# Kernel optimization log

Measured on AMD Instinct MI355X. Metric: run time of the kernel, lower is better.

Reference implementation:

```python
import jax, jax.numpy as jnp
import numpy as np

N = 50000      # nodes
E = 400000     # lower-adjacency edges (avg degree 8)
D = 128        # input_dim == output_dim (o_dim in DEC_HOGNN)
GEO = 20       # geo_dim
H = 3          # heads
C = 128        # out_channels per head
NUM_LAYERS = 3


def _lin_init(key, fan_in, fan_out, extra=()):
    s = 1.0 / np.sqrt(fan_in)
    return jax.random.uniform(key, extra + (fan_in, fan_out), jnp.float32, -s, s)


def setup_inputs() -> dict:
    key = jax.random.key(0)
    ks = jax.random.split(key, 20)
    inp = {
        "h": jax.random.normal(ks[0], (N, D), jnp.float32),
        "lower_adj_feat": jax.random.normal(ks[1], (E, GEO), jnp.float32),
        "dir_w": jax.random.normal(ks[2], (E, 1), jnp.float32),
        "src_idx": jax.random.randint(ks[3], (E,), 0, N),
        "dst_idx": jax.random.randint(ks[4], (E,), 0, N),
        # edge_encoder: Linear(2*D + geo + 1 -> D)
        "W_ee": _lin_init(ks[5], 2 * D + GEO + 1, D),
        "b_ee": jnp.zeros((D,), jnp.float32),
        # residual linear (layer 0 only; others Identity)
        "W_res": _lin_init(ks[6], D, D),
        "b_res": jnp.zeros((D,), jnp.float32),
        # 3 TransformerConv layers, all in=D out=C heads=H (stacked)
        "Wq": _lin_init(ks[7], D, H * C, (NUM_LAYERS,)),
        "bq": jnp.zeros((NUM_LAYERS, H * C), jnp.float32),
        "Wk": _lin_init(ks[8], D, H * C, (NUM_LAYERS,)),
        "bk": jnp.zeros((NUM_LAYERS, H * C), jnp.float32),
        "Wv": _lin_init(ks[9], D, H * C, (NUM_LAYERS,)),
        "bv": jnp.zeros((NUM_LAYERS, H * C), jnp.float32),
        "We": _lin_init(ks[10], D, H * C, (NUM_LAYERS,)),
        "be": jnp.zeros((NUM_LAYERS, H * C), jnp.float32),
        # lin_skip: in -> out_channels (concat=False)
        "Ws": _lin_init(ks[11], D, C, (NUM_LAYERS,)),
        "bs": jnp.zeros((NUM_LAYERS, C), jnp.float32),
        # ctr_lin: Linear(input_dim + output_dim -> output_dim)
        "W_ctr": _lin_init(ks[12], 2 * D, D),
        "b_ctr": jnp.zeros((D,), jnp.float32),
    }
    return inp


def _transformer_conv(x, src, dst, e_attr, Wq, bq, Wk, bk, Wv, bv, We, be, Ws, bs):
    """PyG TransformerConv, heads=H, concat=False (head mean), root skip."""
    n = x.shape[0]
    q = (x @ Wq + bq).reshape(n, H, C)
    k = (x @ Wk + bk).reshape(n, H, C)
    v = (x @ Wv + bv).reshape(n, H, C)
    e = (e_attr @ We + be).reshape(-1, H, C)      # [E,H,C]
    ke = k[src] + e                                # edge-conditioned keys
    alpha = (q[dst] * ke).sum(-1) / jnp.sqrt(jnp.asarray(C, x.dtype))  # [E,H]
    # segment softmax over destination nodes
    amax = jax.ops.segment_max(alpha, dst, num_segments=n)
    amax = jnp.where(jnp.isfinite(amax), amax, 0.0)
    ex = jnp.exp(alpha - amax[dst])
    den = jax.ops.segment_sum(ex, dst, num_segments=n)
    w = ex / (den[dst] + 1e-16)
    msg = (v[src] + e) * w[:, :, None]             # [E,H,C]
    out = jax.ops.segment_sum(msg.reshape(-1, H * C), dst, num_segments=n)
    out = out.reshape(n, H, C).mean(axis=1)        # concat=False -> head mean
    return out + x @ Ws + bs                       # root weight skip


def reference(h, lower_adj_feat, dir_w, src_idx, dst_idx,
              W_ee, b_ee, W_res, b_res,
              Wq, bq, Wk, bk, Wv, bv, We, be, Ws, bs,
              W_ctr, b_ctr):
    # edge encoder: [h[dst], h[src]*dir, dir, geo] -> D
    edge_features = jnp.concatenate(
        [h[dst_idx], h[src_idx] * dir_w, dir_w, lower_adj_feat], axis=-1)
    edge_attr = edge_features @ W_ee + b_ee
    h_cur = h
    for i in range(NUM_LAYERS):
        residual = (h_cur @ W_res + b_res) if i == 0 else h_cur
        h_t = _transformer_conv(h_cur, src_idx, dst_idx, edge_attr,
                                Wq[i], bq[i], Wk[i], bk[i], Wv[i], bv[i],
                                We[i], be[i], Ws[i], bs[i])
        h_cur = jax.nn.relu(h_t + residual)
    return jnp.concatenate([h, h_cur], axis=-1) @ W_ctr + b_ctr
```

## Files before the change

### kernel.cpp

```cpp
#include <hip/hip_runtime.h>
#include <math.h>

#define NN 50000
#define NE 400000

typedef _Float16 f16;
typedef _Float16 f16x8 __attribute__((ext_vector_type(8)));
typedef _Float16 f16x4 __attribute__((ext_vector_type(4)));
typedef _Float16 f16x2 __attribute__((ext_vector_type(2)));
typedef float f32x4 __attribute__((ext_vector_type(4)));

static __device__ __forceinline__ float dot8(f16x8 a, f16x8 b, float acc) {
#if defined(__has_builtin) && __has_builtin(__builtin_amdgcn_fdot2)
#pragma unroll
  for (int j = 0; j < 4; ++j) {
    f16x2 x = {a[2 * j], a[2 * j + 1]};
    f16x2 y = {b[2 * j], b[2 * j + 1]};
    acc = __builtin_amdgcn_fdot2(x, y, acc, false);
  }
#else
#pragma unroll
  for (int j = 0; j < 8; ++j) acc += (float)a[j] * (float)b[j];
#endif
  return acc;
}

#if defined(__has_builtin) && __has_builtin(__builtin_amdgcn_global_load_lds)
#define HAVE_GLL 1
static __device__ __forceinline__ void gload_lds16(const f16* gp, f16* lp) {
  __builtin_amdgcn_global_load_lds((const __attribute__((address_space(1))) void*)gp,
                                   (__attribute__((address_space(3))) void*)lp, 16, 0, 0);
}
#else
#define HAVE_GLL 0
#endif

__global__ __launch_bounds__(256) void hgemm_k128_kernel(
    const f16* __restrict__ A, int lda,
    const f16* __restrict__ WT,
    const float* __restrict__ bias,
    f16* __restrict__ outb, int ldb,
    int M, int ntiles)
{
  __shared__ f16 As[128 * 128];
  __shared__ f16 Bs[64 * 128];
  const int t = threadIdx.x;
  const int wv = t >> 6, lane = t & 63;
  const int l15 = lane & 15, l4 = lane >> 4;
  const int c8 = lane & 15, rsub = lane >> 4;
  const int row0 = blockIdx.x * 128;

#if HAVE_GLL
#pragma unroll
  for (int k = 0; k < 8; ++k) {
    int r = wv * 4 + k * 16 + rsub;
    int rc = row0 + r; if (rc >= M) rc = M - 1;
    const f16* gp = A + (size_t)rc * lda + ((c8 ^ (r & 15)) << 3);
    gload_lds16(gp, As + (wv * 4 + k * 16) * 128);
  }
#else
  for (int i = t; i < 2048; i += 256) {
    int r = i >> 4, cc = i & 15;
    int gr = row0 + r; if (gr >= M) gr = M - 1;
    float4 v = *(const float4*)(A + (size_t)gr * lda + cc * 8);
    *(float4*)(As + r * 128 + ((cc ^ (r & 15)) << 3)) = v;
  }
#endif
  for (int ct = 0; ct < ntiles; ++ct) {
    const int col0 = (blockIdx.y * ntiles + ct) * 64;
#if HAVE_GLL
#pragma unroll
    for (int k = 0; k < 4; ++k) {
      int c = wv * 4 + k * 16 + rsub;
      const f16* gp = WT + (size_t)(col0 + c) * 128 + ((c8 ^ (c & 15)) << 3);
      gload_lds16(gp, Bs + (wv * 4 + k * 16) * 128);
    }
#else
    for (int i = t; i < 1024; i += 256) {
      int c = i >> 4, cc = i & 15;
      float4 v = *(const float4*)(WT + (size_t)(col0 + c) * 128 + cc * 8);
      *(float4*)(Bs + c * 128 + ((cc ^ (c & 15)) << 3)) = v;
    }
#endif
    __syncthreads();
    f32x4 acc[2][4];
#pragma unroll
    for (int m = 0; m < 2; ++m)
#pragma unroll
      for (int n = 0; n < 4; ++n) acc[m][n] = (f32x4){0.f, 0.f, 0.f, 0.f};
#pragma unroll
    for (int ks = 0; ks < 4; ++ks) {
      const int co = (((ks * 4 + l4) ^ l15) << 3);
      f16x8 a0 = *(const f16x8*)(As + (wv * 32 +      l15) * 128 + co);
      f16x8 a1 = *(const f16x8*)(As + (wv * 32 + 16 + l15) * 128 + co);
      f16x8 b0 = *(const f16x8*)(Bs + (     l15) * 128 + co);
      f16x8 b1 = *(const f16x8*)(Bs + (16 + l15) * 128 + co);
      f16x8 b2 = *(const f16x8*)(Bs + (32 + l15) * 128 + co);
      f16x8 b3 = *(const f16x8*)(Bs + (48 + l15) * 128 + co);
      acc[0][0] = __builtin_amdgcn_mfma_f32_16x16x32_f16(a0, b0, acc[0][0], 0, 0, 0);
      acc[0][1] = __builtin_amdgcn_mfma_f32_16x16x32_f16(a0, b1, acc[0][1], 0, 0, 0);
      acc[0][2] = __builtin_amdgcn_mfma_f32_16x16x32_f16(a0, b2, acc[0][2], 0, 0, 0);
      acc[0][3] = __builtin_amdgcn_mfma_f32_16x16x32_f16(a0, b3, acc[0][3], 0, 0, 0);
      acc[1][0] = __builtin_amdgcn_mfma_f32_16x16x32_f16(a1, b0, acc[1][0], 0, 0, 0);
      acc[1][1] = __builtin_amdgcn_mfma_f32_16x16x32_f16(a1, b1, acc[1][1], 0, 0, 0);
      acc[1][2] = __builtin_amdgcn_mfma_f32_16x16x32_f16(a1, b2, acc[1][2], 0, 0, 0);
      acc[1][3] = __builtin_amdgcn_mfma_f32_16x16x32_f16(a1, b3, acc[1][3], 0, 0, 0);
    }
    __syncthreads();
    float bv4[4];
#pragma unroll
    for (int n = 0; n < 4; ++n) bv4[n] = bias ? bias[col0 + n * 16 + l15] : 0.f;
#pragma unroll
    for (int m = 0; m < 2; ++m) {
#pragma unroll
      for (int j = 0; j < 4; ++j) {
        int r = row0 + wv * 32 + m * 16 + l4 * 4 + j;
        if (r >= M) continue;
#pragma unroll
        for (int n = 0; n < 4; ++n) {
          int c = col0 + n * 16 + l15;
          outb[(size_t)r * ldb + c] = (f16)(acc[m][n][j] + bv4[n]);
        }
      }
    }
  }
}

__global__ __launch_bounds__(256) void hgemm2_kernel(
    const f16* __restrict__ A, int lda,
    const f16* __restrict__ A2, int lda2, int a2k,
    const f16* __restrict__ WT, int K,
    const float* __restrict__ bias,
    f16* __restrict__ outb, int ldb,
    const f16* __restrict__ fresid, int ldr,
    int dorelu, int M,
    const f16* __restrict__ ctrW, const float* __restrict__ ctrB,
    float* __restrict__ ctrOut)
{
  __shared__ f16 As[128 * 128];
  __shared__ f16 Bs[128 * 128];
  const int t = threadIdx.x;
  const int wv = t >> 6, lane = t & 63;
  const int l15 = lane & 15, l4 = lane >> 4;
  const int c8 = lane & 15, rsub = lane >> 4;
  const int row0 = blockIdx.x * 128;
  const int col0 = blockIdx.y * 128;

  f32x4 acc[2][8];
#pragma unroll
  for (int m = 0; m < 2; ++m)
#pragma unroll
    for (int n = 0; n < 8; ++n) acc[m][n] = (f32x4){0.f, 0.f, 0.f, 0.f};

  for (int kc = 0; kc < K; kc += 128) {
    const f16* Ap; int koff, ldA;
    if (kc >= a2k) { Ap = A2; koff = kc - a2k; ldA = lda2; }
    else           { Ap = A;  koff = kc;       ldA = lda;  }
#if HAVE_GLL
#pragma unroll
    for (int k = 0; k < 8; ++k) {
      int r = wv * 4 + k * 16 + rsub;
      int rc = row0 + r; if (rc >= M) rc = M - 1;
      const f16* gp = Ap + (size_t)rc * ldA + koff + ((c8 ^ (r & 15)) << 3);
      gload_lds16(gp, As + (wv * 4 + k * 16) * 128);
    }
#pragma unroll
    for (int k = 0; k < 8; ++k) {
      int c = wv * 4 + k * 16 + rsub;
      const f16* gp = WT + (size_t)(col0 + c) * K + kc + ((c8 ^ (c & 15)) << 3);
      gload_lds16(gp, Bs + (wv * 4 + k * 16) * 128);
    }
#else
    for (int i = t; i < 2048; i += 256) {
      int r = i >> 4, cc = i & 15;
      int gr = row0 + r; if (gr >= M) gr = M - 1;
      float4 v = *(const float4*)(Ap + (size_t)gr * ldA + koff + cc * 8);
      *(float4*)(As + r * 128 + ((cc ^ (r & 15)) << 3)) = v;
    }
    for (int i = t; i < 2048; i += 256) {
      int c = i >> 4, cc = i & 15;
      float4 v = *(const float4*)(WT + (size_t)(col0 + c) * K + kc + cc * 8);
      *(float4*)(Bs + c * 128 + ((cc ^ (c & 15)) << 3)) = v;
    }
#endif
    __syncthreads();
#pragma unroll
    for (int ks = 0; ks < 4; ++ks) {
      const int co = (((ks * 4 + l4) ^ l15) << 3);
      f16x8 a0 = *(const f16x8*)(As + (wv * 32 +      l15) * 128 + co);
      f16x8 a1 = *(const f16x8*)(As + (wv * 32 + 16 + l15) * 128 + co);
#pragma unroll
      for (int n = 0; n < 8; ++n) {
        f16x8 b = *(const f16x8*)(Bs + (n * 16 + l15) * 128 + co);
        acc[0][n] = __builtin_amdgcn_mfma_f32_16x16x32_f16(a0, b, acc[0][n], 0, 0, 0);
        acc[1][n] = __builtin_amdgcn_mfma_f32_16x16x32_f16(a1, b, acc[1][n], 0, 0, 0);
      }
    }
    __syncthreads();
  }

  float bv8[8];
#pragma unroll
  for (int n = 0; n < 8; ++n) bv8[n] = bias ? bias[col0 + n * 16 + l15] : 0.f;
#pragma unroll
  for (int m = 0; m < 2; ++m) {
#pragma unroll
    for (int j = 0; j < 4; ++j) {
      int rl = wv * 32 + m * 16 + l4 * 4 + j;
      int r = row0 + rl;
#pragma unroll
      for (int n = 0; n < 8; ++n) {
        int c = col0 + n * 16 + l15;
        float val = acc[m][n][j] + bv8[n];
        if (fresid) val += (float)fresid[(size_t)r * ldr + c];
        if (dorelu) val = fmaxf(val, 0.f);
        f16 hv = (f16)val;
        if (r < M) outb[(size_t)r * ldb + c] = hv;
        if (ctrOut)
          As[rl * 128 + (((c >> 3) ^ (rl & 15)) << 3) + (c & 7)] = hv;
      }
    }
  }

  if (ctrOut) {
    for (int i = t; i < 2048; i += 256) {
      int c = i >> 4, k8 = i & 15;
      float4 v = *(const float4*)(ctrW + (size_t)c * 256 + k8 * 8);
      *(float4*)(Bs + c * 128 + ((k8 ^ (c & 15)) << 3)) = v;
    }
    __syncthreads();
    f32x4 acc2[2][8];
#pragma unroll
    for (int m = 0; m < 2; ++m)
#pragma unroll
      for (int n = 0; n < 8; ++n) acc2[m][n] = (f32x4){0.f, 0.f, 0.f, 0.f};
#pragma unroll
    for (int ks = 0; ks < 4; ++ks) {
      const int co = (((ks * 4 + l4) ^ l15) << 3);
      f16x8 a0 = *(const f16x8*)(As + (wv * 32 +      l15) * 128 + co);
      f16x8 a1 = *(const f16x8*)(As + (wv * 32 + 16 + l15) * 128 + co);
#pragma unroll
      for (int n = 0; n < 8; ++n) {
        f16x8 b = *(const f16x8*)(Bs + (n * 16 + l15) * 128 + co);
        acc2[0][n] = __builtin_amdgcn_mfma_f32_16x16x32_f16(a0, b, acc2[0][n], 0, 0, 0);
        acc2[1][n] = __builtin_amdgcn_mfma_f32_16x16x32_f16(a1, b, acc2[1][n], 0, 0, 0);
      }
    }
    __syncthreads();
    for (int i = t; i < 2048; i += 256) {
      int r = i >> 4, k8 = i & 15;
      int gr = row0 + r; if (gr >= M) gr = M - 1;
      float4 v = *(const float4*)(A2 + (size_t)gr * lda2 + 128 + k8 * 8);
      *(float4*)(As + r * 128 + ((k8 ^ (r & 15)) << 3)) = v;
    }
    for (int i = t; i < 2048; i += 256) {
      int c = i >> 4, k8 = i & 15;
      float4 v = *(const float4*)(ctrW + (size_t)c * 256 + 128 + k8 * 8);
      *(float4*)(Bs + c * 128 + ((k8 ^ (c & 15)) << 3)) = v;
    }
    __syncthreads();
#pragma unroll
    for (int ks = 0; ks < 4; ++ks) {
      const int co = (((ks * 4 + l4) ^ l15) << 3);
      f16x8 a0 = *(const f16x8*)(As + (wv * 32 +      l15) * 128 + co);
      f16x8 a1 = *(const f16x8*)(As + (wv * 32 + 16 + l15) * 128 + co);
#pragma unroll
      for (int n = 0; n < 8; ++n) {
        f16x8 b = *(const f16x8*)(Bs + (n * 16 + l15) * 128 + co);
        acc2[0][n] = __builtin_amdgcn_mfma_f32_16x16x32_f16(a0, b, acc2[0][n], 0, 0, 0);
        acc2[1][n] = __builtin_amdgcn_mfma_f32_16x16x32_f16(a1, b, acc2[1][n], 0, 0, 0);
      }
    }
#pragma unroll
    for (int m = 0; m < 2; ++m) {
#pragma unroll
      for (int j = 0; j < 4; ++j) {
        int r = row0 + wv * 32 + m * 16 + l4 * 4 + j;
        if (r >= M) continue;
#pragma unroll
        for (int n = 0; n < 8; ++n) {
          int c = n * 16 + l15;
          ctrOut[(size_t)r * 128 + c] = acc2[m][n][j] + ctrB[c];
        }
      }
    }
  }
}

__global__ void zero_int_kernel(int* __restrict__ p, int n) {
  int i = blockIdx.x * 256 + threadIdx.x;
  if (i < n) p[i] = 0;
}
__global__ void hist_kernel(const int* __restrict__ dst, int* __restrict__ deg) {
  int e = blockIdx.x * 256 + threadIdx.x;
  if (e < NE) atomicAdd(&deg[dst[e]], 1);
}
__global__ void scanA_kernel(const int* __restrict__ deg, int* __restrict__ rowstart,
                             int* __restrict__ part) {
  __shared__ int sd[256];
  int b = blockIdx.x, t = threadIdx.x, i = b * 256 + t;
  sd[t] = (i < NN) ? deg[i] : 0;
  __syncthreads();
  for (int o = 1; o < 256; o <<= 1) {
    int v = (t >= o) ? sd[t - o] : 0;
    __syncthreads();
    sd[t] += v;
    __syncthreads();
  }
  if (i < NN) rowstart[i + 1] = sd[t];
  if (t == 255) part[b] = sd[255];
}
__global__ void scanB_kernel(int* __restrict__ part, int nb) {
  __shared__ int sd[256];
  int t = threadIdx.x;
  sd[t] = (t < nb) ? part[t] : 0;
  __syncthreads();
  for (int o = 1; o < 256; o <<= 1) {
    int v = (t >= o) ? sd[t - o] : 0;
    __syncthreads();
    sd[t] += v;
    __syncthreads();
  }
  if (t < nb) part[t] = sd[t];
}
__global__ void scanC_kernel(const int* __restrict__ deg, int* __restrict__ rowstart,
                             const int* __restrict__ part, int* __restrict__ cursor) {
  int b = blockIdx.x, t = threadIdx.x, i = b * 256 + t;
  if (i >= NN) return;
  int off = b ? part[b - 1] : 0;
  int fin = rowstart[i + 1] + off;
  rowstart[i + 1] = fin;
  cursor[i] = fin - deg[i];
  if (i == 0) rowstart[0] = 0;
}
__global__ void scatter_kernel(const int* __restrict__ dst, const int* __restrict__ src,
                               const float* __restrict__ dirw, const float* __restrict__ geo,
                               int* __restrict__ cursor,
                               int* __restrict__ srcp, f16* __restrict__ dirpb,
                               f16* __restrict__ geop) {
  int e = blockIdx.x * 256 + threadIdx.x;
  if (e < NE) {
    int pos = atomicAdd(&cursor[dst[e]], 1);
    srcp[pos] = src[e];
    float dv = dirw[e];
    dirpb[pos] = (f16)dv;
    f16* gp = geop + (size_t)pos * 24;
#pragma unroll
    for (int j = 0; j < 20; ++j) gp[j] = (f16)geo[(size_t)e * 20 + j];
    gp[20] = (f16)dv;
    gp[21] = (f16)0.f; gp[22] = (f16)0.f; gp[23] = (f16)0.f;
  }
}

__global__ void prep_kernel(const float* __restrict__ Wee, const float* __restrict__ bee,
                            const float* __restrict__ WeAll, const float* __restrict__ beAll,
                            float* __restrict__ matsAll)
{
  const int layer = blockIdx.y;
  const float* We = WeAll + (size_t)layer * 49152;
  const float* be = beAll + (size_t)layer * 384;
  float* mats = matsAll + (size_t)layer * 132352;
  int idx = blockIdx.x * 256 + threadIdx.x;
  if (idx >= 132352) return;
  float acc = 0.0f;
  if (idx < 49152) {
    int h = idx >> 14, rem = idx & 16383, c = rem >> 7, u = rem & 127;
    for (int j = 0; j < 128; ++j)
      acc += We[(size_t)j * 384 + h * 128 + c] * Wee[(size_t)(128 + u) * 128 + j];
    mats[idx] = acc;
  } else if (idx < 58368) {
    int r = idx - 49152; int h = r / 3072; int rem = r - h * 3072; int c = rem / 24; int u = rem - c * 24;
    if (u < 21) {
      int trow = (u < 20) ? (257 + u) : 256;
      for (int j = 0; j < 128; ++j)
        acc += We[(size_t)j * 384 + h * 128 + c] * Wee[(size_t)trow * 128 + j];
    }
    mats[idx] = acc;
  } else if (idx < 107520) {
    int r = idx - 58368; int h = r >> 14; int rem = r & 16383; int tt = rem >> 7; int c = rem & 127;
    for (int j = 0; j < 128; ++j)
      acc += Wee[(size_t)(128 + tt) * 128 + j] * We[(size_t)j * 384 + h * 128 + c];
    mats[idx] = acc;
  } else if (idx < 115584) {
    int r = idx - 107520; int h = r / 2688; int rem = r - h * 2688; int tt = rem >> 7; int c = rem & 127;
    int trow = (tt < 20) ? (257 + tt) : 256;
    for (int j = 0; j < 128; ++j)
      acc += Wee[(size_t)trow * 128 + j] * We[(size_t)j * 384 + h * 128 + c];
    mats[idx] = acc;
  } else if (idx < 115968) {
    int r = idx - 115584; int h = r >> 7; int c = r & 127;
    for (int j = 0; j < 128; ++j)
      acc += bee[j] * We[(size_t)j * 384 + h * 128 + c];
    mats[idx] = acc + be[h * 128 + c];
  } else {
    int r = idx - 115968; int tt = r >> 7; int c = r & 127;
    for (int j = 0; j < 128; ++j)
      acc += Wee[(size_t)tt * 128 + j] *
             (We[(size_t)j * 384 + c] + We[(size_t)j * 384 + 128 + c] + We[(size_t)j * 384 + 256 + c]);
    mats[idx] = acc * (1.0f / 3.0f);
  }
}

__global__ void prepB_kernel(const float* __restrict__ Wq, const float* __restrict__ bq,
                             const float* __restrict__ Wk, const float* __restrict__ matsAll,
                             f16* __restrict__ WABT, float* __restrict__ biasAB)
{
  int idx = blockIdx.x * 256 + threadIdx.x;
  if (idx < 344064) {
    int i = idx / 114688; int r = idx % 114688; int c = r >> 7; int k = r & 127;
    float acc = 0.f;
    if (c < 384) {
      int h = c >> 7, u = c & 127;
      const float* wq = Wq + ((size_t)i * 128 + k) * 384 + h * 128;
      const float* wk = Wk + ((size_t)i * 128 + u) * 384 + h * 128;
      for (int c2 = 0; c2 < 128; ++c2) acc += wq[c2] * wk[c2];
    } else if (c < 768) {
      int h = (c - 384) >> 7, u = (c - 384) & 127;
      const float* wq = Wq + ((size_t)i * 128 + k) * 384 + h * 128;
      const float* m2 = matsAll + (size_t)i * 132352 + h * 16384 + u;
      for (int c2 = 0; c2 < 128; ++c2) acc += wq[c2] * m2[c2 * 128];
    } else if (c < 840) {
      int h = (c - 768) / 24, tt = (c - 768) % 24;
      const float* wq = Wq + ((size_t)i * 128 + k) * 384 + h * 128;
      const float* m34 = matsAll + (size_t)i * 132352 + 49152 + h * 3072 + tt;
      for (int c2 = 0; c2 < 128; ++c2) acc += wq[c2] * m34[c2 * 24];
    }
    WABT[(size_t)i * 114688 + c * 128 + k] = (f16)acc;
  } else if (idx < 346752) {
    int r = idx - 344064; int i = r / 896; int c = r % 896;
    float acc = 0.f;
    if (c < 384) {
      int h = c >> 7, u = c & 127;
      const float* bqv = bq + i * 384 + h * 128;
      const float* wk = Wk + ((size_t)i * 128 + u) * 384 + h * 128;
      for (int c2 = 0; c2 < 128; ++c2) acc += bqv[c2] * wk[c2];
    } else if (c < 768) {
      int h = (c - 384) >> 7, u = (c - 384) & 127;
      const float* bqv = bq + i * 384 + h * 128;
      const float* m2 = matsAll + (size_t)i * 132352 + h * 16384 + u;
      for (int c2 = 0; c2 < 128; ++c2) acc += bqv[c2] * m2[c2 * 128];
    } else if (c < 840) {
      int h = (c - 768) / 24, tt = (c - 768) % 24;
      const float* bqv = bq + i * 384 + h * 128;
      const float* m34 = matsAll + (size_t)i * 132352 + 49152 + h * 3072 + tt;
      for (int c2 = 0; c2 < 128; ++c2) acc += bqv[c2] * m34[c2 * 24];
    }
    biasAB[i * 896 + c] = acc;
  }
}

__global__ void prep2_kernel(const float* __restrict__ matsAll, const float* __restrict__ Wv,
                             const float* __restrict__ bv, const float* __restrict__ Ws,
                             const float* __restrict__ Wres, f16* __restrict__ W2bigT)
{
  int idx = blockIdx.x * 256 + threadIdx.x;
  if (idx >= 442368) return;
  int i = idx / 147456; int r = idx % 147456; int c = r / 1152; int k = r % 1152;
  float v = 0.f;
  if (k < 384) {
    int h = k >> 7, tt = k & 127;
    v = matsAll[(size_t)i * 132352 + 58368 + h * 16384 + tt * 128 + c];
  } else if (k < 768) {
    int h = (k - 384) >> 7, u = (k - 384) & 127;
    v = Wv[((size_t)i * 128 + u) * 384 + h * 128 + c];
  } else if (k < 840) {
    int h = (k - 768) / 24, tt = (k - 768) % 24;
    if (tt < 21)       v = matsAll[(size_t)i * 132352 + 107520 + h * 2688 + tt * 128 + c];
    else if (tt == 21) v = matsAll[(size_t)i * 132352 + 115584 + h * 128 + c]
                         + bv[i * 384 + h * 128 + c];
  } else if (k < 896) {
    v = 0.f;
  } else if (k < 1024) {
    v = matsAll[(size_t)i * 132352 + 115968 + (k - 896) * 128 + c];
  } else {
    v = Ws[((size_t)i * 128 + (k - 1024)) * 128 + c];
    if (i == 0) v += Wres[(k - 1024) * 128 + c];
  }
  W2bigT[(size_t)i * 147456 + c * 1152 + k] = (f16)v;
}

__global__ void wprep_kernel(const float* __restrict__ Wctr, const float* __restrict__ bs,
                             const float* __restrict__ bres,
                             f16* __restrict__ WctrT2, float* __restrict__ bias0)
{
  int idx = blockIdx.x * 256 + threadIdx.x;
  if (idx < 32768) {
    int c = idx >> 8, k = idx & 255;
    float v = (k < 128) ? Wctr[(size_t)(128 + k) * 128 + c]
                        : Wctr[(size_t)(k - 128) * 128 + c];
    WctrT2[idx] = (f16)v;
  } else if (idx < 32896) {
    int c = idx - 32768;
    bias0[c] = bs[c] + bres[c];
  }
}

__global__ __launch_bounds__(256) void attn_kernel(
    const f16* __restrict__ xh,
    f16* __restrict__ nbuf,
    const int* __restrict__ rowstart,
    const int* __restrict__ srcp,
    const f16* __restrict__ dirpb,
    const f16* __restrict__ geop)
{
  const int sl = threadIdx.x & 15;
  const int n = blockIdx.x * 16 + (threadIdx.x >> 4);
  const float rsC = 0.088388347648318447f;
  f16* row = nbuf + (size_t)n * 1024;

  f16x8 qk[3], g2[3];
#pragma unroll
  for (int h = 0; h < 3; ++h) {
    qk[h] = *(const f16x8*)(row + h * 128 + sl * 8);
    g2[h] = *(const f16x8*)(row + 384 + h * 128 + sl * 8);
  }
  float g34a[3], g34c[3];
#pragma unroll
  for (int h = 0; h < 3; ++h) {
    g34a[h] = (float)row[768 + h * 24 + sl];
    g34c[h] = (sl < 8) ? (float)row[768 + h * 24 + 16 + sl] : 0.f;
  }
  float den[3] = {0.f, 0.f, 0.f};
  float F2[3][8], Fv[3][8];
#pragma unroll
  for (int h = 0; h < 3; ++h)
#pragma unroll
    for (int j = 0; j < 8; ++j) { F2[h][j] = 0.f; Fv[h][j] = 0.f; }
  float f34a[3] = {0.f, 0.f, 0.f}, f34c[3] = {0.f, 0.f, 0.f};

  const int beg = rowstart[n], end = rowstart[n + 1];
  int ii = beg;
  for (; ii + 1 < end; ii += 2) {
    const int s0 = srcp[ii], s1 = srcp[ii + 1];
    const float d0 = (float)dirpb[ii], d1 = (float)dirpb[ii + 1];
    const f16* p0 = xh + (size_t)s0 * 256 + sl * 8;
    const f16* p1 = xh + (size_t)s1 * 256 + sl * 8;
    f16x8 xv0 = *(const f16x8*)p0;
    f16x8 hv0 = *(const f16x8*)(p0 + 128);
    f16x8 xv1 = *(const f16x8*)p1;
    f16x8 hv1 = *(const f16x8*)(p1 + 128);
    const float gea0 = (float)geop[(size_t)ii * 24 + sl];
    const float geb0 = (sl < 8) ? (float)geop[(size_t)ii * 24 + 16 + sl] : 0.f;
    const float gea1 = (float)geop[(size_t)(ii + 1) * 24 + sl];
    const float geb1 = (sl < 8) ? (float)geop[(size_t)(ii + 1) * 24 + 16 + sl] : 0.f;

    float pa[6];
#pragma unroll
    for (int h = 0; h < 3; ++h) {
      pa[h]     = dot8(qk[h], xv0, 0.f) + d0 * dot8(g2[h], hv0, 0.f)
                + gea0 * g34a[h] + geb0 * g34c[h];
      pa[3 + h] = dot8(qk[h], xv1, 0.f) + d1 * dot8(g2[h], hv1, 0.f)
                + gea1 * g34a[h] + geb1 * g34c[h];
    }
#pragma unroll
    for (int off = 1; off < 16; off <<= 1) {
#pragma unroll
      for (int q = 0; q < 6; ++q) pa[q] += __shfl_xor(pa[q], off);
    }
    float w0[3], w1[3];
#pragma unroll
    for (int h = 0; h < 3; ++h) {
      w0[h] = __expf(pa[h] * rsC);
      w1[h] = __expf(pa[3 + h] * rsC);
      den[h] += w0[h] + w1[h];
    }
#pragma unroll
    for (int h = 0; h < 3; ++h) {
      const float wd0 = w0[h] * d0, wd1 = w1[h] * d1;
#pragma unroll
      for (int j = 0; j < 8; ++j) {
        F2[h][j] = fmaf(wd0, (float)hv0[j], fmaf(wd1, (float)hv1[j], F2[h][j]));
        Fv[h][j] = fmaf(w0[h], (float)xv0[j], fmaf(w1[h], (float)xv1[j], Fv[h][j]));
      }
      f34a[h] = fmaf(w0[h], gea0, fmaf(w1[h], gea1, f34a[h]));
      f34c[h] = fmaf(w0[h], geb0, fmaf(w1[h], geb1, f34c[h]));
    }
  }
  if (ii < end) {
    const int s0 = srcp[ii];
    const float d0 = (float)dirpb[ii];
    const f16* p0 = xh + (size_t)s0 * 256 + sl * 8;
    f16x8 xv0 = *(const f16x8*)p0;
    f16x8 hv0 = *(const f16x8*)(p0 + 128);
    const float gea0 = (float)geop[(size_t)ii * 24 + sl];
    const float geb0 = (sl < 8) ? (float)geop[(size_t)ii * 24 + 16 + sl] : 0.f;
    float pa[3];
#pragma unroll
    for (int h = 0; h < 3; ++h)
      pa[h] = dot8(qk[h], xv0, 0.f) + d0 * dot8(g2[h], hv0, 0.f)
            + gea0 * g34a[h] + geb0 * g34c[h];
#pragma unroll
    for (int off = 1; off < 16; off <<= 1) {
#pragma unroll
      for (int q = 0; q < 3; ++q) pa[q] += __shfl_xor(pa[q], off);
    }
#pragma unroll
    for (int h = 0; h < 3; ++h) {
      const float w = __expf(pa[h] * rsC);
      den[h] += w;
      const float wd = w * d0;
#pragma unroll
      for (int j = 0; j < 8; ++j) {
        F2[h][j] = fmaf(wd, (float)hv0[j], F2[h][j]);
        Fv[h][j] = fmaf(w, (float)xv0[j], Fv[h][j]);
      }
      f34a[h] = fmaf(w, gea0, f34a[h]);
      f34c[h] = fmaf(w, geb0, f34c[h]);
    }
  }

  float sc[3], swh[3];
#pragma unroll
  for (int h = 0; h < 3; ++h) {
    sc[h] = (1.f / 3.f) / (den[h] + 1e-16f);
    swh[h] = den[h] * sc[h];
  }
#pragma unroll
  for (int h = 0; h < 3; ++h) {
    f16x8 o1, o2;
#pragma unroll
    for (int j = 0; j < 8; ++j) {
      o1[j] = (f16)(F2[h][j] * sc[h]);
      o2[j] = (f16)(Fv[h][j] * sc[h]);
    }
    *(f16x8*)(row + h * 128 + sl * 8) = o1;
    *(f16x8*)(row + 384 + h * 128 + sl * 8) = o2;
  }
#pragma unroll
  for (int h = 0; h < 3; ++h) {
    row[768 + h * 24 + sl] = (f16)(f34a[h] * sc[h]);
    if (sl < 8) {
      float fcv = (sl == 5) ? swh[h] : f34c[h] * sc[h];
      row[768 + h * 24 + 16 + sl] = (f16)fcv;
    }
  }
  f16x8 ho = *(const f16x8*)(xh + (size_t)n * 256 + 128 + sl * 8);
  if (beg >= end) {
#pragma unroll
    for (int j = 0; j < 8; ++j) ho[j] = (f16)0.f;
  }
  *(f16x8*)(row + 896 + sl * 8) = ho;
}

__global__ void hconv_kernel(const float* __restrict__ src, f16* __restrict__ xh) {
  int i = blockIdx.x * 256 + threadIdx.x;
  if (i >= NN * 32) return;
  float4 a = ((const float4*)src)[i];
  f16x4 o;
  o[0] = (f16)a.x; o[1] = (f16)a.y; o[2] = (f16)a.z; o[3] = (f16)a.w;
  int r = i >> 5, c4 = i & 31;
  *(f16x4*)(xh + (size_t)r * 256 + c4 * 4) = o;
  *(f16x4*)(xh + (size_t)r * 256 + 128 + c4 * 4) = o;
}

extern "C" void kernel_launch(void* const* d_in, const int* in_sizes, int n_in,
                              void* d_out, int out_size, void* d_ws, size_t ws_size,
                              hipStream_t stream)
{
  (void)in_sizes; (void)n_in; (void)out_size; (void)ws_size;
  const float* h    = (const float*)d_in[0];
  const float* geo  = (const float*)d_in[1];
  const float* dirw = (const float*)d_in[2];
  const int*   src  = (const int*)d_in[3];
  const int*   dst  = (const int*)d_in[4];
  const float* Wee  = (const float*)d_in[5];
  const float* bee  = (const float*)d_in[6];
  const float* Wres = (const float*)d_in[7];
  const float* bres = (const float*)d_in[8];
  const float* Wq   = (const float*)d_in[9];
  const float* bq   = (const float*)d_in[10];
  const float* Wk   = (const float*)d_in[11];
  const float* bk   = (const float*)d_in[12];  (void)bk;
  const float* Wv   = (const float*)d_in[13];
  const float* bv   = (const float*)d_in[14];
  const float* We   = (const float*)d_in[15];
  const float* be   = (const float*)d_in[16];
  const float* Ws   = (const float*)d_in[17];
  const float* bs   = (const float*)d_in[18];
  const float* Wctr = (const float*)d_in[19];
  const float* bctr = (const float*)d_in[20];

  char* base = (char*)d_ws;
  size_t off = 0;
  auto take = [&](size_t bytes) -> char* {
    char* p = base + off;
    off += bytes;
    off = (off + 255) & ~(size_t)255;
    return p;
  };
  f16* nbuf     = (f16*)take((size_t)NN * 1024 * 2);
  f16* xh       = (f16*)take((size_t)NN * 256 * 2);
  float* mats   = (float*)take((size_t)3 * 132352 * 4);
  f16* WABT     = (f16*)take((size_t)3 * 114688 * 2);
  float* biasAB = (float*)take((size_t)3 * 896 * 4);
  f16* W2bigT   = (f16*)take((size_t)3 * 147456 * 2);
  f16* WctrT2   = (f16*)take(32768 * 2);
  float* bias0  = (float*)take(128 * 4);
  f16* dirpb    = (f16*)take((size_t)NE * 2);
  f16* geop     = (f16*)take((size_t)NE * 24 * 2);
  int* deg      = (int*)take((size_t)NN * 4);
  int* rowstart = (int*)take((size_t)(NN + 1) * 4);
  int* cursor   = (int*)take((size_t)NN * 4);
  int* srcp     = (int*)take((size_t)NE * 4);
  int* part     = (int*)take(256 * 4);

  zero_int_kernel<<<(NN + 255) / 256, 256, 0, stream>>>(deg, NN);
  hist_kernel<<<(NE + 255) / 256, 256, 0, stream>>>(dst, deg);
  scanA_kernel<<<196, 256, 0, stream>>>(deg, rowstart, part);
  scanB_kernel<<<1, 256, 0, stream>>>(part, 196);
  scanC_kernel<<<196, 256, 0, stream>>>(deg, rowstart, part, cursor);
  scatter_kernel<<<(NE + 255) / 256, 256, 0, stream>>>(dst, src, dirw, geo, cursor,
                                                       srcp, dirpb, geop);
  hconv_kernel<<<6250, 256, 0, stream>>>(h, xh);
  wprep_kernel<<<129, 256, 0, stream>>>(Wctr, bs, bres, WctrT2, bias0);
  prep_kernel<<<dim3(518, 3), 256, 0, stream>>>(Wee, bee, We, be, mats);
  prepB_kernel<<<(346752 + 255) / 256, 256, 0, stream>>>(Wq, bq, Wk, mats, WABT, biasAB);
  prep2_kernel<<<(442368 + 255) / 256, 256, 0, stream>>>(mats, Wv, bv, Ws, Wres, W2bigT);

  for (int i = 0; i < 3; ++i) {
    hgemm_k128_kernel<<<dim3(391, 2), 256, 0, stream>>>(xh, 256, WABT + (size_t)i * 114688,
        biasAB + (size_t)i * 896, nbuf, 1024, NN, 7);
    attn_kernel<<<3125, 256, 0, stream>>>(xh, nbuf, rowstart, srcp, dirpb, geop);
    const float* obias = (i == 0) ? bias0 : (bs + i * 128);
    const f16* resid = (i == 0) ? nullptr : xh;
    const f16* ctrW = (i == 2) ? WctrT2 : nullptr;
    const float* ctrB = (i == 2) ? bctr : nullptr;
    float* ctrOut = (i == 2) ? (float*)d_out : nullptr;
    hgemm2_kernel<<<dim3(391, 1), 256, 0, stream>>>(nbuf, 1024, xh, 256, 1024,
        W2bigT + (size_t)i * 147456, 1152, obias, xh, 256,
        resid, 256, 1, NN, ctrW, ctrB, ctrOut);
  }
}
```

Before: 602.5 us.

## Compute weight-folding prep products with MFMA GEMMs instead of scalar loops

Replaces the scalar per-thread weight-precomputation kernels (prep_kernel, prepB_kernel) with an fp16 conversion pass, two small MFMA-based GEMM launches (pgemm_kernel) and gather and bias kernels. The folded Wee·We and Wq·(Wk|M) products are now computed on matrix cores from fp16 copies. This is meant to cut the cost of the long serial dot-product loops in the setup phase. In exchange the intermediate matrices are held in fp16 rather than fp32, which adds rounding error, and the setup now needs more launches.

```diff
diff --git a/kernel.cpp b/kernel.cpp
--- a/kernel.cpp
+++ b/kernel.cpp
@@ -126,6 +126,108 @@
   }
 }
 
+__global__ __launch_bounds__(256) void pgemm_kernel(
+    const f16* __restrict__ Abase, const f16* __restrict__ Wbase,
+    f16* __restrict__ Obase, int mode)
+{
+  __shared__ f16 As[128 * 128];
+  __shared__ f16 Bs[64 * 128];
+  const int t = threadIdx.x;
+  const int wv = t >> 6, lane = t & 63;
+  const int l15 = lane & 15, l4 = lane >> 4;
+  const int c8 = lane & 15, rsub = lane >> 4;
+  const int row0 = blockIdx.x * 128;
+  const int z = blockIdx.z;
+  const f16* A; const f16* WT; int ldw, ntiles, ih = 0, hh = 0;
+  f16* Os;
+  if (mode == 0) {
+    A = Abase; WT = Wbase + (size_t)z * 49152; ldw = 128;
+    Os = Obase + (size_t)z * 147456; ntiles = 3;
+  } else {
+    ih = z / 3; hh = z % 3;
+    A = Abase + (size_t)z * 49152;
+    WT = Wbase + (size_t)ih * 49152 + hh * 128; ldw = 384;
+    Os = Obase + (size_t)ih * 114688; ntiles = 1;
+  }
+#if HAVE_GLL
+#pragma unroll
+  for (int k = 0; k < 8; ++k) {
+    int r = wv * 4 + k * 16 + rsub;
+    const f16* gp = A + (size_t)(row0 + r) * 128 + ((c8 ^ (r & 15)) << 3);
+    gload_lds16(gp, As + (wv * 4 + k * 16) * 128);
+  }
+#else
+  for (int i = t; i < 2048; i += 256) {
+    int r = i >> 4, cc = i & 15;
+    float4 v = *(const float4*)(A + (size_t)(row0 + r) * 128 + cc * 8);
+    *(float4*)(As + r * 128 + ((cc ^ (r & 15)) << 3)) = v;
+  }
+#endif
+  for (int ct = 0; ct < ntiles; ++ct) {
+    const int col0 = (blockIdx.y * ntiles + ct) * 64;
+#if HAVE_GLL
+#pragma unroll
+    for (int k = 0; k < 4; ++k) {
+      int c = wv * 4 + k * 16 + rsub;
+      const f16* gp = WT + (size_t)(col0 + c) * ldw + ((c8 ^ (c & 15)) << 3);
+      gload_lds16(gp, Bs + (wv * 4 + k * 16) * 128);
+    }
+#else
+    for (int i = t; i < 1024; i += 256) {
+      int c = i >> 4, cc = i & 15;
+      float4 v = *(const float4*)(WT + (size_t)(col0 + c) * ldw + cc * 8);
+      *(float4*)(Bs + c * 128 + ((cc ^ (c & 15)) << 3)) = v;
+    }
+#endif
+    __syncthreads();
+    f32x4 acc[2][4];
+#pragma unroll
+    for (int m = 0; m < 2; ++m)
+#pragma unroll
+      for (int n = 0; n < 4; ++n) acc[m][n] = (f32x4){0.f, 0.f, 0.f, 0.f};
+#pragma unroll
+    for (int ks = 0; ks < 4; ++ks) {
+      const int co = (((ks * 4 + l4) ^ l15) << 3);
+      f16x8 a0 = *(const f16x8*)(As + (wv * 32 +      l15) * 128 + co);
+      f16x8 a1 = *(const f16x8*)(As + (wv * 32 + 16 + l15) * 128 + co);
+      f16x8 b0 = *(const f16x8*)(Bs + (     l15) * 128 + co);
+      f16x8 b1 = *(const f16x8*)(Bs + (16 + l15) * 128 + co);
+      f16x8 b2 = *(const f16x8*)(Bs + (32 + l15) * 128 + co);
+      f16x8 b3 = *(const f16x8*)(Bs + (48 + l15) * 128 + co);
+      acc[0][0] = __builtin_amdgcn_mfma_f32_16x16x32_f16(a0, b0, acc[0][0], 0, 0, 0);
+      acc[0][1] = __builtin_amdgcn_mfma_f32_16x16x32_f16(a0, b1, acc[0][1], 0, 0, 0);
+      acc[0][2] = __builtin_amdgcn_mfma_f32_16x16x32_f16(a0, b2, acc[0][2], 0, 0, 0);
+      acc[0][3] = __builtin_amdgcn_mfma_f32_16x16x32_f16(a0, b3, acc[0][3], 0, 0, 0);
+      acc[1][0] = __builtin_amdgcn_mfma_f32_16x16x32_f16(a1, b0, acc[1][0], 0, 0, 0);
+      acc[1][1] = __builtin_amdgcn_mfma_f32_16x16x32_f16(a1, b1, acc[1][1], 0, 0, 0);
+      acc[1][2] = __builtin_amdgcn_mfma_f32_16x16x32_f16(a1, b2, acc[1][2], 0, 0, 0);
+      acc[1][3] = __builtin_amdgcn_mfma_f32_16x16x32_f16(a1, b3, acc[1][3], 0, 0, 0);
+    }
+    __syncthreads();
+#pragma unroll
+    for (int m = 0; m < 2; ++m) {
+#pragma unroll
+      for (int j = 0; j < 4; ++j) {
+        int r = row0 + wv * 32 + m * 16 + l4 * 4 + j;
+#pragma unroll
+        for (int n = 0; n < 4; ++n) {
+          int cc = col0 + n * 16 + l15;
+          f16 v = (f16)acc[m][n][j];
+          if (mode == 0) {
+            Os[(size_t)r * 384 + cc] = v;
+          } else if (r < 280) {
+            int c;
+            if (r < 128)      c = hh * 128 + r;
+            else if (r < 256) c = 384 + hh * 128 + (r - 128);
+            else              c = 768 + hh * 24 + (r - 256);
+            Os[(size_t)c * 128 + cc] = v;
+          }
+        }
+      }
+    }
+  }
+}
+
 __global__ __launch_bounds__(256) void hgemm2_kernel(
     const f16* __restrict__ A, int lda,
     const f16* __restrict__ A2, int lda2, int a2k,
@@ -352,126 +454,96 @@
   }
 }
 
-__global__ void prep_kernel(const float* __restrict__ Wee, const float* __restrict__ bee,
-                            const float* __restrict__ WeAll, const float* __restrict__ beAll,
-                            float* __restrict__ matsAll)
-{
-  const int layer = blockIdx.y;
-  const float* We = WeAll + (size_t)layer * 49152;
-  const float* be = beAll + (size_t)layer * 384;
-  float* mats = matsAll + (size_t)layer * 132352;
+__global__ void convert_kernel(const float* __restrict__ Wee, const float* __restrict__ bee,
+                               const float* __restrict__ WeAll, const float* __restrict__ Wq,
+                               const float* __restrict__ Wk,
+                               f16* __restrict__ Vf, f16* __restrict__ WeT,
+                               f16* __restrict__ Wq16, f16* __restrict__ Wk16)
+{
   int idx = blockIdx.x * 256 + threadIdx.x;
-  if (idx >= 132352) return;
-  float acc = 0.0f;
   if (idx < 49152) {
-    int h = idx >> 14, rem = idx & 16383, c = rem >> 7, u = rem & 127;
-    for (int j = 0; j < 128; ++j)
-      acc += We[(size_t)j * 384 + h * 128 + c] * Wee[(size_t)(128 + u) * 128 + j];
-    mats[idx] = acc;
-  } else if (idx < 58368) {
-    int r = idx - 49152; int h = r / 3072; int rem = r - h * 3072; int c = rem / 24; int u = rem - c * 24;
-    if (u < 21) {
-      int trow = (u < 20) ? (257 + u) : 256;
-      for (int j = 0; j < 128; ++j)
-        acc += We[(size_t)j * 384 + h * 128 + c] * Wee[(size_t)trow * 128 + j];
-    }
-    mats[idx] = acc;
-  } else if (idx < 107520) {
-    int r = idx - 58368; int h = r >> 14; int rem = r & 16383; int tt = rem >> 7; int c = rem & 127;
-    for (int j = 0; j < 128; ++j)
-      acc += Wee[(size_t)(128 + tt) * 128 + j] * We[(size_t)j * 384 + h * 128 + c];
-    mats[idx] = acc;
-  } else if (idx < 115584) {
-    int r = idx - 107520; int h = r / 2688; int rem = r - h * 2688; int tt = rem >> 7; int c = rem & 127;
-    int trow = (tt < 20) ? (257 + tt) : 256;
-    for (int j = 0; j < 128; ++j)
-      acc += Wee[(size_t)trow * 128 + j] * We[(size_t)j * 384 + h * 128 + c];
-    mats[idx] = acc;
-  } else if (idx < 115968) {
-    int r = idx - 115584; int h = r >> 7; int c = r & 127;
-    for (int j = 0; j < 128; ++j)
-      acc += bee[j] * We[(size_t)j * 384 + h * 128 + c];
-    mats[idx] = acc + be[h * 128 + c];
-  } else {
-    int r = idx - 115968; int tt = r >> 7; int c = r & 127;
-    for (int j = 0; j < 128; ++j)
-      acc += Wee[(size_t)tt * 128 + j] *
-             (We[(size_t)j * 384 + c] + We[(size_t)j * 384 + 128 + c] + We[(size_t)j * 384 + 256 + c]);
-    mats[idx] = acc * (1.0f / 3.0f);
-  }
-}
-
-__global__ void prepB_kernel(const float* __restrict__ Wq, const float* __restrict__ bq,
-                             const float* __restrict__ Wk, const float* __restrict__ matsAll,
-                             f16* __restrict__ WABT, float* __restrict__ biasAB)
+    int r = idx >> 7, j = idx & 127;
+    float v = 0.f;
+    if (r < 128)       v = Wee[(size_t)(128 + r) * 128 + j];
+    else if (r < 256)  v = Wee[(size_t)(r - 128) * 128 + j];
+    else if (r < 276)  v = Wee[(size_t)(257 + (r - 256)) * 128 + j];
+    else if (r == 276) v = Wee[(size_t)256 * 128 + j];
+    else if (r == 277) v = bee[j];
+    Vf[idx] = (f16)v;
+  } else if (idx < 196608) {
+    int rr = idx - 49152; int i = rr / 49152; int r2 = rr % 49152;
+    int cc = r2 >> 7, j = r2 & 127;
+    WeT[rr] = (f16)WeAll[((size_t)i * 128 + j) * 384 + cc];
+  } else if (idx < 344064) {
+    int rr = idx - 196608;
+    Wq16[rr] = (f16)Wq[rr];
+  } else if (idx < 491520) {
+    int rr = idx - 344064;
+    Wk16[rr] = (f16)Wk[rr];
+  }
+}
+
+__global__ void arows_kernel(const f16* __restrict__ Wk16, const f16* __restrict__ Sall,
+                             f16* __restrict__ Arows)
 {
   int idx = blockIdx.x * 256 + threadIdx.x;
-  if (idx < 344064) {
-    int i = idx / 114688; int r = idx % 114688; int c = r >> 7; int k = r & 127;
-    float acc = 0.f;
-    if (c < 384) {
-      int h = c >> 7, u = c & 127;
-      const float* wq = Wq + ((size_t)i * 128 + k) * 384 + h * 128;
-      const float* wk = Wk + ((size_t)i * 128 + u) * 384 + h * 128;
-      for (int c2 = 0; c2 < 128; ++c2) acc += wq[c2] * wk[c2];
-    } else if (c < 768) {
-      int h = (c - 384) >> 7, u = (c - 384) & 127;
-      const float* wq = Wq + ((size_t)i * 128 + k) * 384 + h * 128;
-      const float* m2 = matsAll + (size_t)i * 132352 + h * 16384 + u;
-      for (int c2 = 0; c2 < 128; ++c2) acc += wq[c2] * m2[c2 * 128];
-    } else if (c < 840) {
-      int h = (c - 768) / 24, tt = (c - 768) % 24;
-      const float* wq = Wq + ((size_t)i * 128 + k) * 384 + h * 128;
-      const float* m34 = matsAll + (size_t)i * 132352 + 49152 + h * 3072 + tt;
-      for (int c2 = 0; c2 < 128; ++c2) acc += wq[c2] * m34[c2 * 24];
-    }
-    WABT[(size_t)i * 114688 + c * 128 + k] = (f16)acc;
-  } else if (idx < 346752) {
-    int r = idx - 344064; int i = r / 896; int c = r % 896;
-    float acc = 0.f;
-    if (c < 384) {
-      int h = c >> 7, u = c & 127;
-      const float* bqv = bq + i * 384 + h * 128;
-      const float* wk = Wk + ((size_t)i * 128 + u) * 384 + h * 128;
-      for (int c2 = 0; c2 < 128; ++c2) acc += bqv[c2] * wk[c2];
-    } else if (c < 768) {
-      int h = (c - 384) >> 7, u = (c - 384) & 127;
-      const float* bqv = bq + i * 384 + h * 128;
-      const float* m2 = matsAll + (size_t)i * 132352 + h * 16384 + u;
-      for (int c2 = 0; c2 < 128; ++c2) acc += bqv[c2] * m2[c2 * 128];
-    } else if (c < 840) {
-      int h = (c - 768) / 24, tt = (c - 768) % 24;
-      const float* bqv = bq + i * 384 + h * 128;
-      const float* m34 = matsAll + (size_t)i * 132352 + 49152 + h * 3072 + tt;
-      for (int c2 = 0; c2 < 128; ++c2) acc += bqv[c2] * m34[c2 * 24];
-    }
-    biasAB[i * 896 + c] = acc;
-  }
-}
-
-__global__ void prep2_kernel(const float* __restrict__ matsAll, const float* __restrict__ Wv,
-                             const float* __restrict__ bv, const float* __restrict__ Ws,
-                             const float* __restrict__ Wres, f16* __restrict__ W2bigT)
+  if (idx >= 442368) return;
+  int z = idx / 49152; int rr = idx % 49152; int r = rr >> 7; int k2 = rr & 127;
+  int i = z / 3, h = z % 3;
+  f16 v = (f16)0.f;
+  if (r < 128)       v = Wk16[(size_t)i * 49152 + (size_t)r * 384 + h * 128 + k2];
+  else if (r < 256)  v = Sall[(size_t)i * 147456 + (size_t)(r - 128) * 384 + h * 128 + k2];
+  else if (r < 277)  v = Sall[(size_t)i * 147456 + (size_t)r * 384 + h * 128 + k2];
+  Arows[idx] = v;
+}
+
+__global__ void biasAB_kernel(const f16* __restrict__ Arows, const float* __restrict__ bq,
+                              float* __restrict__ biasAB)
+{
+  int idx = blockIdx.x * 256 + threadIdx.x;
+  if (idx >= 2688) return;
+  int i = idx / 896, c = idx % 896;
+  float acc = 0.f;
+  int h = 0, ro = -1;
+  if (c < 384)      { h = c >> 7;         ro = c & 127; }
+  else if (c < 768) { h = (c - 384) >> 7; ro = 128 + ((c - 384) & 127); }
+  else if (c < 840) { h = (c - 768) / 24; ro = 256 + ((c - 768) % 24); }
+  if (ro >= 0) {
+    const f16* ar = Arows + ((size_t)(i * 3 + h)) * 49152 + (size_t)ro * 128;
+    const float* bqh = bq + i * 384 + h * 128;
+    for (int k2 = 0; k2 < 128; ++k2) acc += (float)ar[k2] * bqh[k2];
+  }
+  biasAB[idx] = acc;
+}
+
+__global__ void prep2_kernel(const f16* __restrict__ Sall, const float* __restrict__ beAll,
+                             const float* __restrict__ Wv, const float* __restrict__ bv,
+                             const float* __restrict__ Ws, const float* __restrict__ Wres,
+                             f16* __restrict__ W2bigT)
 {
   int idx = blockIdx.x * 256 + threadIdx.x;
   if (idx >= 442368) return;
   int i = idx / 147456; int r = idx % 147456; int c = r / 1152; int k = r % 1152;
+  const f16* S = Sall + (size_t)i * 147456;
   float v = 0.f;
   if (k < 384) {
     int h = k >> 7, tt = k & 127;
-    v = matsAll[(size_t)i * 132352 + 58368 + h * 16384 + tt * 128 + c];
+    v = (float)S[(size_t)tt * 384 + h * 128 + c];
   } else if (k < 768) {
     int h = (k - 384) >> 7, u = (k - 384) & 127;
     v = Wv[((size_t)i * 128 + u) * 384 + h * 128 + c];
   } else if (k < 840) {
     int h = (k - 768) / 24, tt = (k - 768) % 24;
-    if (tt < 21)       v = matsAll[(size_t)i * 132352 + 107520 + h * 2688 + tt * 128 + c];
-    else if (tt == 21) v = matsAll[(size_t)i * 132352 + 115584 + h * 128 + c]
-                         + bv[i * 384 + h * 128 + c];
+    if (tt < 21)       v = (float)S[(size_t)(256 + tt) * 384 + h * 128 + c];
+    else if (tt == 21) v = (float)S[(size_t)277 * 384 + h * 128 + c]
+                         + beAll[i * 384 + h * 128 + c] + bv[i * 384 + h * 128 + c];
   } else if (k < 896) {
     v = 0.f;
   } else if (k < 1024) {
-    v = matsAll[(size_t)i * 132352 + 115968 + (k - 896) * 128 + c];
+    int tt = k - 896;
+    v = ((float)S[(size_t)(128 + tt) * 384 + c]
+       + (float)S[(size_t)(128 + tt) * 384 + 128 + c]
+       + (float)S[(size_t)(128 + tt) * 384 + 256 + c]) * (1.0f / 3.0f);
   } else {
     v = Ws[((size_t)i * 128 + (k - 1024)) * 128 + c];
     if (i == 0) v += Wres[(k - 1024) * 128 + c];
@@ -690,7 +762,12 @@
   };
   f16* nbuf     = (f16*)take((size_t)NN * 1024 * 2);
   f16* xh       = (f16*)take((size_t)NN * 256 * 2);
-  float* mats   = (float*)take((size_t)3 * 132352 * 4);
+  f16* Vf16     = (f16*)take(49152 * 2);
+  f16* WeT16    = (f16*)take((size_t)3 * 49152 * 2);
+  f16* Wq16     = (f16*)take((size_t)3 * 49152 * 2);
+  f16* Wk16     = (f16*)take((size_t)3 * 49152 * 2);
+  f16* Sall     = (f16*)take((size_t)3 * 147456 * 2);
+  f16* Arows    = (f16*)take((size_t)9 * 49152 * 2);
   f16* WABT     = (f16*)take((size_t)3 * 114688 * 2);
   float* biasAB = (float*)take((size_t)3 * 896 * 4);
   f16* W2bigT   = (f16*)take((size_t)3 * 147456 * 2);
@@ -713,9 +790,14 @@
                                                        srcp, dirpb, geop);
   hconv_kernel<<<6250, 256, 0, stream>>>(h, xh);
   wprep_kernel<<<129, 256, 0, stream>>>(Wctr, bs, bres, WctrT2, bias0);
-  prep_kernel<<<dim3(518, 3), 256, 0, stream>>>(Wee, bee, We, be, mats);
-  prepB_kernel<<<(346752 + 255) / 256, 256, 0, stream>>>(Wq, bq, Wk, mats, WABT, biasAB);
-  prep2_kernel<<<(442368 + 255) / 256, 256, 0, stream>>>(mats, Wv, bv, Ws, Wres, W2bigT);
+
+  convert_kernel<<<(491520 + 255) / 256, 256, 0, stream>>>(Wee, bee, We, Wq, Wk,
+                                                           Vf16, WeT16, Wq16, Wk16);
+  pgemm_kernel<<<dim3(3, 2, 3), 256, 0, stream>>>(Vf16, WeT16, Sall, 0);
+  arows_kernel<<<(442368 + 255) / 256, 256, 0, stream>>>(Wk16, Sall, Arows);
+  pgemm_kernel<<<dim3(3, 2, 9), 256, 0, stream>>>(Arows, Wq16, WABT, 1);
+  biasAB_kernel<<<11, 256, 0, stream>>>(Arows, bq, biasAB);
+  prep2_kernel<<<(442368 + 255) / 256, 256, 0, stream>>>(Sall, be, Wv, bv, Ws, Wres, W2bigT);
 
   for (int i = 0; i < 3; ++i) {
     hgemm_k128_kernel<<<dim3(391, 2), 256, 0, stream>>>(xh, 256, WABT + (size_t)i * 114688,
```

New measurement: 569.6 us. 1.06x faster.
